# Performance work log

Hardware: AMD Instinct MI355X
Metric: run time of the kernel (lower is better)

Reference implementation:

```python
import jax, jax.numpy as jnp
import numpy as np

B, N, IN_C, HID_C, OUT_C = 8, 2048, 128, 256, 32


def setup_inputs() -> dict:
    key = jax.random.key(0)
    ks = jax.random.split(key, 8)
    s1 = 1.0 / np.sqrt(IN_C)
    s2 = 1.0 / np.sqrt(HID_C)
    return {
        "x": jax.random.normal(ks[0], (B, N, IN_C), dtype=jnp.float32),
        "A": jax.random.randint(ks[1], (B, N, N), 0, 2, dtype=jnp.int32),
        "W1_l": jax.random.normal(ks[2], (IN_C, HID_C), dtype=jnp.float32) * s1,
        "W1_r": jax.random.normal(ks[3], (IN_C, HID_C), dtype=jnp.float32) * s1,
        "b1": jnp.zeros((HID_C,), dtype=jnp.float32),
        "W2_l": jax.random.normal(ks[4], (HID_C, OUT_C), dtype=jnp.float32) * s2,
        "W2_r": jax.random.normal(ks[5], (HID_C, OUT_C), dtype=jnp.float32) * s2,
        "b2": jnp.zeros((OUT_C,), dtype=jnp.float32),
    }


def _mean_agg(mask, deg_inv, h):
    # edge (i, j) means source i -> target j (PyG source_to_target flow):
    # agg[b, j] = mean over i with A[b, i, j] != 0 of h[b, i]
    return jnp.einsum("bij,bid->bjd", mask, h) * deg_inv


def reference(x, A, W1_l, W1_r, b1, W2_l, W2_r, b2):
    mask = (A != 0).astype(x.dtype)            # [B, N, N]
    deg = jnp.sum(mask, axis=1)                # in-degree per target node, [B, N]
    deg_inv = (1.0 / jnp.maximum(deg, 1.0))[..., None]  # isolated nodes -> 0 agg

    # SAGEConv 1: lin_l(mean_agg(x)) + lin_r(x) + bias, then ReLU
    # (dropout p=0.2 is inactive in eval mode)
    h = _mean_agg(mask, deg_inv, x) @ W1_l + x @ W1_r + b1
    h = jax.nn.relu(h)

    # SAGEConv 2
    out = _mean_agg(mask, deg_inv, h) @ W2_l + h @ W2_r + b2  # [B, N, OUT_C]
    return (jax.nn.log_softmax(out, axis=-1), out)
```

## Files before the change

### kernel.cpp

```cpp
#include <hip/hip_runtime.h>


#define B_   8
#define N_   2048
#define INC  128
#define HID  256
#define OUTC 32

typedef __attribute__((ext_vector_type(8))) __bf16 bf16x8;
typedef __attribute__((ext_vector_type(4))) float f32x4;
typedef __attribute__((ext_vector_type(4))) unsigned int u32x4;
typedef __attribute__((ext_vector_type(2))) unsigned int u32x2;

__device__ __forceinline__ unsigned short f2bf(float f) {
  unsigned int u = __float_as_uint(f);
  u += 0x7FFFu + ((u >> 16) & 1u);
  return (unsigned short)(u >> 16);
}

__device__ __forceinline__ f32x4 mfma16(bf16x8 a, bf16x8 b, f32x4 c) {
  return __builtin_amdgcn_mfma_f32_16x16x32_bf16(a, b, c, 0, 0, 0);
}

__device__ __forceinline__ bf16x8 ones_frag() {
  union { unsigned short u[8]; bf16x8 v; } o;
#pragma unroll
  for (int i = 0; i < 8; i++) o.u[i] = 0x3F80;
  return o.v;
}

__device__ __forceinline__ void lut_init(u32x2* lut, int t) {
  if (t < 16) {
    unsigned int w0 = (t & 1 ? 0x3F80u : 0u) | (t & 2 ? 0x3F800000u : 0u);
    unsigned int w1 = (t & 4 ? 0x3F80u : 0u) | (t & 8 ? 0x3F800000u : 0u);
    u32x2 e = {w0, w1};
    lut[t] = e;
  }
}

__device__ __forceinline__ bf16x8 expand8(const u32x2* lut, unsigned int bval) {
  union { u32x2 u2[2]; bf16x8 v; } af;
  af.u2[0] = lut[bval & 15u];
  af.u2[1] = lut[bval >> 4];
  return af.v;
}

__global__ __launch_bounds__(256, 8) void k_prep(
    const int* __restrict__ A, const float* __restrict__ x,
    const float* __restrict__ W1l, const float* __restrict__ W1r,
    const float* __restrict__ W2l, const float* __restrict__ W2r,
    unsigned int* __restrict__ bits, unsigned short* __restrict__ xT,
    unsigned short* __restrict__ xcat,
    unsigned short* __restrict__ W1cT, unsigned short* __restrict__ W2cT) {
  __shared__ unsigned short xls[128 * 72];
  const int bx = blockIdx.x, t = threadIdx.x;
  if (bx < 2048) {
    const int w = t >> 6, l = t & 63;
    const int b = bx & 7, tile4 = bx >> 3;
    const int gw2 = tile4 * 4 + w;
    const int it = gw2 >> 5, jt = gw2 & 31;
    const int i0 = it * 64, j0 = jt * 64;
    const int* Ap = A + ((size_t)(b * N_) + i0) * N_ + j0 + l;
    unsigned long long col = 0;
#pragma unroll 8
    for (int r = 0; r < 64; r++) {
      int a = Ap[(size_t)r * N_];
      unsigned long long m = __ballot(a != 0);
      col |= ((m >> l) & 1ull) << r;
    }
    *reinterpret_cast<unsigned long long*>(
        bits + ((size_t)(b * N_) + j0 + l) * 64 + (i0 >> 5)) = col;
  } else if (bx < 2304) {
    const int bb = bx - 2048;
    const int b = bb & 7, it = bb >> 3;
    const int i0 = it * 64;
    const int dq = (t & 31) * 4;
    const int irow = t >> 5;
#pragma unroll
    for (int s = 0; s < 8; s++) {
      int il = s * 8 + irow;
      int i = i0 + il;
      f32x4 v = *reinterpret_cast<const f32x4*>(x + ((size_t)(b * N_ + i)) * INC + dq);
      unsigned int p0 = f2bf(v[0]) | ((unsigned int)f2bf(v[1]) << 16);
      unsigned int p1 = f2bf(v[2]) | ((unsigned int)f2bf(v[3]) << 16);
      u32x2 pk = {p0, p1};
      *reinterpret_cast<u32x2*>(xcat + ((size_t)(b * N_ + i)) * INC + dq) = pk;
      xls[(dq + 0) * 72 + il] = f2bf(v[0]);
      xls[(dq + 1) * 72 + il] = f2bf(v[1]);
      xls[(dq + 2) * 72 + il] = f2bf(v[2]);
      xls[(dq + 3) * 72 + il] = f2bf(v[3]);
    }
    __syncthreads();
    const int d = t >> 1, half = t & 1;
    const u32x4* src = reinterpret_cast<const u32x4*>(&xls[d * 72 + half * 32]);
    u32x4* dst = reinterpret_cast<u32x4*>(xT + ((size_t)(b * INC + d)) * N_ + i0 + half * 32);
#pragma unroll
    for (int q = 0; q < 4; q++) dst[q] = src[q];
  } else if (bx < 2368) {
    int base = (bx - 2304) * 1024 + t * 4;
#pragma unroll
    for (int q = 0; q < 4; q++) {
      int id = base + q;
      int e = id >> 8, k = id & 255;
      float v = (k < 128) ? W1l[k * 256 + e] : W1r[(k - 128) * 256 + e];
      W1cT[id] = f2bf(v);
    }
  } else {
    int base = (bx - 2368) * 1024 + t * 4;
#pragma unroll
    for (int q = 0; q < 4; q++) {
      int id = base + q;
      int n = id >> 8, k = id & 255;
      float v = (n < 32) ? W2l[k * 32 + n] : W2r[k * 32 + (n - 32)];
      W2cT[id] = f2bf(v);
    }
  }
}

__global__ __launch_bounds__(256, 2) void k_fused1(
    const unsigned int* __restrict__ bits, const unsigned short* __restrict__ xT,
    const unsigned short* __restrict__ xcat,
    const unsigned short* __restrict__ W1cT, const unsigned short* __restrict__ W2cT,
    const float* __restrict__ b1, const float* __restrict__ b2,
    unsigned short* __restrict__ hlT, float* __restrict__ hr,
    float* __restrict__ deg_inv) {
  __shared__ u32x2 lut[16];
  __shared__ __align__(16) float pdeg[4][2][16][4];
  __shared__ __align__(16) unsigned short acat_s[32 * 264];
  union SU {
    float part[4][6][2][64][4];
    unsigned short hs[32 * 264];
  };
  __shared__ __align__(16) SU su;

  const int t = threadIdx.x;
  const int w = t >> 6, l = t & 63, lr = l & 15, lq = l >> 4;
  lut_init(lut, t);

  const int b = blockIdx.x & 7, j0 = (blockIdx.x >> 3) * 32;

  const int xr = t >> 3, xs = t & 7;
  const unsigned short* xp = xcat + ((size_t)(b * N_ + j0 + xr)) * INC + xs * 16;
  u32x4 xpart0 = *reinterpret_cast<const u32x4*>(xp);
  u32x4 xpart1 = *reinterpret_cast<const u32x4*>(xp + 8);

  __syncthreads();

  const unsigned int* bp0 = bits + ((size_t)(b * N_ + j0 + lr)) * 64 + w * 16;
  const unsigned int* bp1 = bp0 + (size_t)16 * 64;
  const unsigned short* xb = xT + (size_t)b * INC * N_ + w * 512;

  const f32x4 zero = {0.f, 0.f, 0.f, 0.f};
  f32x4 acc[2][8];
#pragma unroll
  for (int jt = 0; jt < 2; jt++)
#pragma unroll
    for (int ds = 0; ds < 8; ds++) acc[jt][ds] = zero;
  f32x4 dacc[2] = {zero, zero};
  const bf16x8 onesf = ones_frag();

  for (int s = 0; s < 16; s++) {
    bf16x8 af0 = expand8(lut, (bp0[s] >> (lq * 8)) & 0xFFu);
    bf16x8 af1 = expand8(lut, (bp1[s] >> (lq * 8)) & 0xFFu);
    dacc[0] = mfma16(af0, onesf, dacc[0]);
    dacc[1] = mfma16(af1, onesf, dacc[1]);
#pragma unroll
    for (int ds = 0; ds < 8; ds++) {
      bf16x8 bfr = *reinterpret_cast<const bf16x8*>(
          xb + ((size_t)(ds * 16 + lr)) * N_ + s * 32 + lq * 8);
      acc[0][ds] = mfma16(af0, bfr, acc[0][ds]);
      acc[1][ds] = mfma16(af1, bfr, acc[1][ds]);
    }
  }

#pragma unroll
  for (int ds = 0; ds < 8; ds++) {
    if ((ds >> 1) != w) {
      int dsi = (ds < 2 * w) ? ds : ds - 2;
#pragma unroll
      for (int jt = 0; jt < 2; jt++)
        *reinterpret_cast<f32x4*>(&su.part[w][dsi][jt][l][0]) = acc[jt][ds];
    }
  }
  if (lr == 0) {
#pragma unroll
    for (int jt = 0; jt < 2; jt++)
      *reinterpret_cast<f32x4*>(&pdeg[w][jt][lq][0]) = dacc[jt];
  }
  *reinterpret_cast<u32x4*>(&acat_s[xr * 264 + 128 + xs * 16]) = xpart0;
  *reinterpret_cast<u32x4*>(&acat_s[xr * 264 + 128 + xs * 16 + 8]) = xpart1;
  __syncthreads();

  float dinv2[2][4];
#pragma unroll
  for (int jt = 0; jt < 2; jt++)
#pragma unroll
    for (int r = 0; r < 4; r++) {
      float deg = pdeg[0][jt][lq][r] + pdeg[1][jt][lq][r] +
                  pdeg[2][jt][lq][r] + pdeg[3][jt][lq][r];
      dinv2[jt][r] = 1.0f / fmaxf(deg, 1.0f);
    }
  if (w < 2 && lr == 0) {
#pragma unroll
    for (int r = 0; r < 4; r++)
      deg_inv[b * N_ + j0 + w * 16 + lq * 4 + r] = dinv2[w][r];
  }
#pragma unroll
  for (int dd = 0; dd < 2; dd++) {
    int ds = 2 * w + dd;
#pragma unroll
    for (int jt = 0; jt < 2; jt++) {
      f32x4 sum = acc[jt][ds];
#pragma unroll
      for (int src = 0; src < 4; src++) {
        if (src != w) {
          int dsi = (ds < 2 * src) ? ds : ds - 2;
          f32x4 p = *reinterpret_cast<f32x4*>(&su.part[src][dsi][jt][l][0]);
          sum += p;
        }
      }
#pragma unroll
      for (int r = 0; r < 4; r++)
        acat_s[(jt * 16 + lq * 4 + r) * 264 + ds * 16 + lr] =
            f2bf(sum[r] * dinv2[jt][r]);
    }
  }
  __syncthreads();

  f32x4 acc2[2][4];
#pragma unroll
  for (int jt = 0; jt < 2; jt++)
#pragma unroll
    for (int es = 0; es < 4; es++) acc2[jt][es] = zero;
  const int e0 = w * 64;
#pragma unroll
  for (int ks = 0; ks < 8; ks++) {
    bf16x8 af0 = *reinterpret_cast<const bf16x8*>(&acat_s[lr * 264 + ks * 32 + lq * 8]);
    bf16x8 af1 = *reinterpret_cast<const bf16x8*>(&acat_s[(16 + lr) * 264 + ks * 32 + lq * 8]);
#pragma unroll
    for (int es = 0; es < 4; es++) {
      bf16x8 bfr = *reinterpret_cast<const bf16x8*>(
          W1cT + ((size_t)(e0 + es * 16 + lr)) * HID + ks * 32 + lq * 8);
      acc2[0][es] = mfma16(af0, bfr, acc2[0][es]);
      acc2[1][es] = mfma16(af1, bfr, acc2[1][es]);
    }
  }
  __syncthreads();
#pragma unroll
  for (int jt = 0; jt < 2; jt++)
#pragma unroll
    for (int es = 0; es < 4; es++) {
      int e = e0 + es * 16 + lr;
      float bias = b1[e];
#pragma unroll
      for (int r = 0; r < 4; r++)
        su.hs[(jt * 16 + lq * 4 + r) * 264 + e] =
            f2bf(fmaxf(acc2[jt][es][r] + bias, 0.0f));
    }
  __syncthreads();

  const int jt = w & 1, nh = w >> 1;
  f32x4 a2[2] = {zero, zero};
#pragma unroll
  for (int ks = 0; ks < 8; ks++) {
    bf16x8 af = *reinterpret_cast<const bf16x8*>(
        &su.hs[(jt * 16 + lr) * 264 + ks * 32 + lq * 8]);
#pragma unroll
    for (int ns = 0; ns < 2; ns++) {
      bf16x8 bfr = *reinterpret_cast<const bf16x8*>(
          W2cT + ((size_t)(nh * 32 + ns * 16 + lr)) * HID + ks * 32 + lq * 8);
      a2[ns] = mfma16(af, bfr, a2[ns]);
    }
  }
  if (nh == 0) {
#pragma unroll
    for (int ns = 0; ns < 2; ns++) {
      int c = ns * 16 + lr;
      unsigned int p0 = f2bf(a2[ns][0]) | ((unsigned int)f2bf(a2[ns][1]) << 16);
      unsigned int p1 = f2bf(a2[ns][2]) | ((unsigned int)f2bf(a2[ns][3]) << 16);
      u32x2 pk = {p0, p1};
      *reinterpret_cast<u32x2*>(
          hlT + ((size_t)(b * 32 + c)) * N_ + j0 + jt * 16 + lq * 4) = pk;
    }
  } else {
#pragma unroll
    for (int ns = 0; ns < 2; ns++) {
      int c = ns * 16 + lr;
      float bias = b2[c];
#pragma unroll
      for (int r = 0; r < 4; r++)
        hr[((size_t)(b * N_ + j0 + jt * 16 + lq * 4 + r)) * OUTC + c] = a2[ns][r] + bias;
    }
  }
}

__global__ __launch_bounds__(256, 2) void k_agg2out(
    const unsigned int* __restrict__ bits, const unsigned short* __restrict__ hlT,
    const float* __restrict__ deg_inv, const float* __restrict__ hr,
    float* __restrict__ out) {
  __shared__ u32x2 lut[16];
  __shared__ __align__(16) float part[4][2][2][64][4];
  const int t = threadIdx.x;
  const int w = t >> 6, l = t & 63, lr = l & 15, lq = l >> 4;
  lut_init(lut, t);
  __syncthreads();
  const int b = blockIdx.x & 7, j0 = (blockIdx.x >> 3) * 32;
  const unsigned int* bp0 = bits + ((size_t)(b * N_ + j0 + lr)) * 64 + w * 16;
  const unsigned int* bp1 = bp0 + (size_t)16 * 64;
  const unsigned short* hb = hlT + (size_t)b * 32 * N_ + w * 512;

  const f32x4 zero = {0.f, 0.f, 0.f, 0.f};
  f32x4 acc[2][2] = {{zero, zero}, {zero, zero}};

  for (int s = 0; s < 16; s++) {
    bf16x8 af0 = expand8(lut, (bp0[s] >> (lq * 8)) & 0xFFu);
    bf16x8 af1 = expand8(lut, (bp1[s] >> (lq * 8)) & 0xFFu);
#pragma unroll
    for (int cs = 0; cs < 2; cs++) {
      bf16x8 bfr = *reinterpret_cast<const bf16x8*>(
          hb + ((size_t)(cs * 16 + lr)) * N_ + s * 32 + lq * 8);
      acc[0][cs] = mfma16(af0, bfr, acc[0][cs]);
      acc[1][cs] = mfma16(af1, bfr, acc[1][cs]);
    }
  }
#pragma unroll
  for (int jt = 0; jt < 2; jt++)
#pragma unroll
    for (int cs = 0; cs < 2; cs++)
      *reinterpret_cast<f32x4*>(&part[w][jt][cs][l][0]) = acc[jt][cs];
  __syncthreads();
  if (w >= 2) return;

  const int jt = w;
  const size_t SZ = (size_t)B_ * N_ * OUTC;
#pragma unroll
  for (int r = 0; r < 4; r++) {
    int j = j0 + jt * 16 + lq * 4 + r;
    float dv = deg_inv[b * N_ + j];
    size_t base = ((size_t)(b * N_ + j)) * OUTC;
    float v0 = (part[0][jt][0][l][r] + part[1][jt][0][l][r] +
                part[2][jt][0][l][r] + part[3][jt][0][l][r]) * dv + hr[base + lr];
    float v1 = (part[0][jt][1][l][r] + part[1][jt][1][l][r] +
                part[2][jt][1][l][r] + part[3][jt][1][l][r]) * dv + hr[base + 16 + lr];
    float m = fmaxf(v0, v1);
#pragma unroll
    for (int d = 1; d < 16; d <<= 1) m = fmaxf(m, __shfl_xor(m, d, 64));
    float s = __expf(v0 - m) + __expf(v1 - m);
#pragma unroll
    for (int d = 1; d < 16; d <<= 1) s += __shfl_xor(s, d, 64);
    float ls = m + __logf(s);
    out[base + lr] = v0 - ls;
    out[base + 16 + lr] = v1 - ls;
    out[SZ + base + lr] = v0;
    out[SZ + base + 16 + lr] = v1;
  }
}

extern "C" void kernel_launch(void* const* d_in, const int* in_sizes, int n_in,
                              void* d_out, int out_size, void* d_ws, size_t ws_size,
                              hipStream_t stream) {
  (void)in_sizes; (void)n_in; (void)out_size; (void)ws_size;
  const float* x   = (const float*)d_in[0];
  const int*   A   = (const int*)d_in[1];
  const float* W1l = (const float*)d_in[2];
  const float* W1r = (const float*)d_in[3];
  const float* b1  = (const float*)d_in[4];
  const float* W2l = (const float*)d_in[5];
  const float* W2r = (const float*)d_in[6];
  const float* b2  = (const float*)d_in[7];
  float* out = (float*)d_out;

  char* ws = (char*)d_ws;
  unsigned short* W1cT    = (unsigned short*)(ws + 0);
  unsigned short* W2cT    = (unsigned short*)(ws + 131072);
  float*          deg_inv = (float*)(ws + 163840);
  unsigned int*   bits    = (unsigned int*)(ws + 229376);
  unsigned short* xT      = (unsigned short*)(ws + 4423680);
  unsigned short* xcat    = (unsigned short*)(ws + 8617984);
  unsigned short* hlT     = (unsigned short*)(ws + 12812288);
  float*          hr      = (float*)(ws + 13860864);

  k_prep   <<<dim3(2384), dim3(256), 0, stream>>>(A, x, W1l, W1r, W2l, W2r,
                                                  bits, xT, xcat, W1cT, W2cT);
  k_fused1 <<<dim3(512),  dim3(256), 0, stream>>>(bits, xT, xcat, W1cT, W2cT,
                                                  b1, b2, hlT, hr, deg_inv);
  k_agg2out<<<dim3(512),  dim3(256), 0, stream>>>(bits, hlT, deg_inv, hr, out);
}
```

Measured before the change: 283.9 us.

## Vectorize adjacency bit-packing and tile xT/hlT into 32-node blocks

The adjacency bit-packing now has each lane read four consecutive int32 columns with one 16-byte load and ballot four times, so each wave covers a 64x256 tile and k_prep launches far fewer blocks. The transposed bf16 feature buffers (xT and hlT) move from a [feature][node] layout to tiles of 32 nodes, so the MFMA B-fragment loads in both aggregation kernels read contiguous 8 KB or 2 KB chunks instead of rows strided by N. This is meant to cut load-instruction count on the 128 MB adjacency read and improve cache and TLB locality in the aggregation loops. The cost is four times the ballot and register work per lane and less block-level parallelism in the packing phase.

```diff
diff --git a/kernel.cpp b/kernel.cpp
--- a/kernel.cpp
+++ b/kernel.cpp
@@ -9,6 +9,7 @@
 
 typedef __attribute__((ext_vector_type(8))) __bf16 bf16x8;
 typedef __attribute__((ext_vector_type(4))) float f32x4;
+typedef __attribute__((ext_vector_type(4))) int i32x4;
 typedef __attribute__((ext_vector_type(4))) unsigned int u32x4;
 typedef __attribute__((ext_vector_type(2))) unsigned int u32x2;
 
@@ -54,24 +55,33 @@
     unsigned short* __restrict__ W1cT, unsigned short* __restrict__ W2cT) {
   __shared__ unsigned short xls[128 * 72];
   const int bx = blockIdx.x, t = threadIdx.x;
-  if (bx < 2048) {
+  if (bx < 512) {
     const int w = t >> 6, l = t & 63;
-    const int b = bx & 7, tile4 = bx >> 3;
-    const int gw2 = tile4 * 4 + w;
-    const int it = gw2 >> 5, jt = gw2 & 31;
-    const int i0 = it * 64, j0 = jt * 64;
-    const int* Ap = A + ((size_t)(b * N_) + i0) * N_ + j0 + l;
-    unsigned long long col = 0;
-#pragma unroll 8
+    const int b = bx & 7, tile = bx >> 3;
+    const int gw = tile * 4 + w;
+    const int it = gw >> 3, jt = gw & 7;
+    const int i0 = it * 64, j0 = jt * 256;
+    const int* Ap = A + ((size_t)(b * N_) + i0) * N_ + j0 + 4 * l;
+    unsigned long long c0 = 0, c1 = 0, c2 = 0, c3 = 0;
+#pragma unroll 4
     for (int r = 0; r < 64; r++) {
-      int a = Ap[(size_t)r * N_];
-      unsigned long long m = __ballot(a != 0);
-      col |= ((m >> l) & 1ull) << r;
-    }
-    *reinterpret_cast<unsigned long long*>(
-        bits + ((size_t)(b * N_) + j0 + l) * 64 + (i0 >> 5)) = col;
-  } else if (bx < 2304) {
-    const int bb = bx - 2048;
+      i32x4 a = *reinterpret_cast<const i32x4*>(Ap + (size_t)r * N_);
+      unsigned long long m0 = __ballot(a[0] != 0);
+      unsigned long long m1 = __ballot(a[1] != 0);
+      unsigned long long m2 = __ballot(a[2] != 0);
+      unsigned long long m3 = __ballot(a[3] != 0);
+      c0 |= ((m0 >> l) & 1ull) << r;
+      c1 |= ((m1 >> l) & 1ull) << r;
+      c2 |= ((m2 >> l) & 1ull) << r;
+      c3 |= ((m3 >> l) & 1ull) << r;
+    }
+    unsigned long long cols[4] = {c0, c1, c2, c3};
+#pragma unroll
+    for (int c = 0; c < 4; c++)
+      *reinterpret_cast<unsigned long long*>(
+          bits + ((size_t)(b * N_) + j0 + 4 * l + c) * 64 + (i0 >> 5)) = cols[c];
+  } else if (bx < 768) {
+    const int bb = bx - 512;
     const int b = bb & 7, it = bb >> 3;
     const int i0 = it * 64;
     const int dq = (t & 31) * 4;
@@ -93,11 +103,12 @@
     __syncthreads();
     const int d = t >> 1, half = t & 1;
     const u32x4* src = reinterpret_cast<const u32x4*>(&xls[d * 72 + half * 32]);
-    u32x4* dst = reinterpret_cast<u32x4*>(xT + ((size_t)(b * INC + d)) * N_ + i0 + half * 32);
+    u32x4* dst = reinterpret_cast<u32x4*>(
+        xT + (((size_t)(b * 64 + it * 2 + half)) * 128 + d) * 32);
 #pragma unroll
     for (int q = 0; q < 4; q++) dst[q] = src[q];
-  } else if (bx < 2368) {
-    int base = (bx - 2304) * 1024 + t * 4;
+  } else if (bx < 832) {
+    int base = (bx - 768) * 1024 + t * 4;
 #pragma unroll
     for (int q = 0; q < 4; q++) {
       int id = base + q;
@@ -106,7 +117,7 @@
       W1cT[id] = f2bf(v);
     }
   } else {
-    int base = (bx - 2368) * 1024 + t * 4;
+    int base = (bx - 832) * 1024 + t * 4;
 #pragma unroll
     for (int q = 0; q < 4; q++) {
       int id = base + q;
@@ -148,7 +159,7 @@
 
   const unsigned int* bp0 = bits + ((size_t)(b * N_ + j0 + lr)) * 64 + w * 16;
   const unsigned int* bp1 = bp0 + (size_t)16 * 64;
-  const unsigned short* xb = xT + (size_t)b * INC * N_ + w * 512;
+  const unsigned short* xb = xT + ((size_t)b * 64 + w * 16) * (128 * 32);
 
   const f32x4 zero = {0.f, 0.f, 0.f, 0.f};
   f32x4 acc[2][8];
@@ -167,7 +178,7 @@
 #pragma unroll
     for (int ds = 0; ds < 8; ds++) {
       bf16x8 bfr = *reinterpret_cast<const bf16x8*>(
-          xb + ((size_t)(ds * 16 + lr)) * N_ + s * 32 + lq * 8);
+          xb + (size_t)s * 4096 + (ds * 16 + lr) * 32 + lq * 8);
       acc[0][ds] = mfma16(af0, bfr, acc[0][ds]);
       acc[1][ds] = mfma16(af1, bfr, acc[1][ds]);
     }
@@ -280,7 +291,7 @@
       unsigned int p1 = f2bf(a2[ns][2]) | ((unsigned int)f2bf(a2[ns][3]) << 16);
       u32x2 pk = {p0, p1};
       *reinterpret_cast<u32x2*>(
-          hlT + ((size_t)(b * 32 + c)) * N_ + j0 + jt * 16 + lq * 4) = pk;
+          hlT + (((size_t)(b * 64 + (j0 >> 5))) * 32 + c) * 32 + jt * 16 + lq * 4) = pk;
     }
   } else {
 #pragma unroll
@@ -307,7 +318,7 @@
   const int b = blockIdx.x & 7, j0 = (blockIdx.x >> 3) * 32;
   const unsigned int* bp0 = bits + ((size_t)(b * N_ + j0 + lr)) * 64 + w * 16;
   const unsigned int* bp1 = bp0 + (size_t)16 * 64;
-  const unsigned short* hb = hlT + (size_t)b * 32 * N_ + w * 512;
+  const unsigned short* hb = hlT + ((size_t)b * 64 + w * 16) * (32 * 32);
 
   const f32x4 zero = {0.f, 0.f, 0.f, 0.f};
   f32x4 acc[2][2] = {{zero, zero}, {zero, zero}};
@@ -318,7 +329,7 @@
 #pragma unroll
     for (int cs = 0; cs < 2; cs++) {
       bf16x8 bfr = *reinterpret_cast<const bf16x8*>(
-          hb + ((size_t)(cs * 16 + lr)) * N_ + s * 32 + lq * 8);
+          hb + s * 1024 + (cs * 16 + lr) * 32 + lq * 8);
       acc[0][cs] = mfma16(af0, bfr, acc[0][cs]);
       acc[1][cs] = mfma16(af1, bfr, acc[1][cs]);
     }
@@ -375,14 +386,14 @@
   unsigned short* W2cT    = (unsigned short*)(ws + 131072);
   float*          deg_inv = (float*)(ws + 163840);
   unsigned int*   bits    = (unsigned int*)(ws + 229376);
-  unsigned short* xT      = (unsigned short*)(ws + 4423680);
+  unsigned short* xTt     = (unsigned short*)(ws + 4423680);
   unsigned short* xcat    = (unsigned short*)(ws + 8617984);
-  unsigned short* hlT     = (unsigned short*)(ws + 12812288);
+  unsigned short* hlTt    = (unsigned short*)(ws + 12812288);
   float*          hr      = (float*)(ws + 13860864);
 
-  k_prep   <<<dim3(2384), dim3(256), 0, stream>>>(A, x, W1l, W1r, W2l, W2r,
-                                                  bits, xT, xcat, W1cT, W2cT);
-  k_fused1 <<<dim3(512),  dim3(256), 0, stream>>>(bits, xT, xcat, W1cT, W2cT,
-                                                  b1, b2, hlT, hr, deg_inv);
-  k_agg2out<<<dim3(512),  dim3(256), 0, stream>>>(bits, hlT, deg_inv, hr, out);
-}
+  k_prep   <<<dim3(848),  dim3(256), 0, stream>>>(A, x, W1l, W1r, W2l, W2r,
+                                                  bits, xTt, xcat, W1cT, W2cT);
+  k_fused1 <<<dim3(512),  dim3(256), 0, stream>>>(bits, xTt, xcat, W1cT, W2cT,
+                                                  b1, b2, hlTt, hr, deg_inv);
+  k_agg2out<<<dim3(512),  dim3(256), 0, stream>>>(bits, hlTt, deg_inv, hr, out);
+}
```

New measurement: 265.5 us. 6.5% less time.
